# Kernel tuning notes

Measured on AMD Instinct MI355X. Metric: run time of the kernel, lower is better.

## Reference

```python
import jax, jax.numpy as jnp
import numpy as np

KS = 3          # kernel_size
DIM = 3         # dimension
B, N = 4, 16384
CMAX = 64       # voxel coordinate range [0, CMAX)
K = KS ** DIM   # kernel_volume = 27
SHIFT = KS      # makes neighbor coords non-negative
BASE = CMAX + 2 * KS  # per-axis encoding base


def _kernel_offsets():
    # matches torch: arange(-ks//2 + 1, ks//2 + 1) per dim, meshgrid 'ij'
    r = jnp.arange(-(KS) // 2 + 1, KS // 2 + 1)
    grid = jnp.meshgrid(*([r] * DIM), indexing='ij')
    return jnp.stack(grid, axis=-1).reshape(-1, DIM)  # [K, DIM]


def setup_inputs() -> dict:
    key = jax.random.key(0)
    k1, _ = jax.random.split(key)
    coordinates = jax.random.randint(k1, (B, N, DIM), 0, CMAX, dtype=jnp.int32)
    batch_indices = jnp.broadcast_to(jnp.arange(B, dtype=jnp.int32)[:, None], (B, N))
    return {"coordinates": coordinates, "batch_indices": batch_indices}


def reference(coordinates, batch_indices):
    """Vectorized kernel-map construction (replaces the Python dict-hash loops).

    Returns:
      in_idx  [B*N*K] : index of the input point within its batch
      out_idx [B*N*K] : dense output index (first-appearance order, matches dict insertion)
      rel_pos [B*N*K] : kernel offset index
      out_key [B*N*K, 3] : unique output coordinates, padded with -1 past num_out
      num_out [] : number of valid unique output keys
    """
    Bv, Nv, D = coordinates.shape
    offsets = _kernel_offsets()            # [K, 3]
    Kv = offsets.shape[0]
    # neighbor coordinates, iteration order (b, idx, k) == torch loop order
    nb = coordinates[:, :, None, :] + offsets[None, None, :, :]  # [B, N, K, 3]
    c = nb + SHIFT                                               # non-negative
    b_ids = batch_indices[:, :, None].astype(jnp.int32)
    keys = (b_ids * (BASE ** 3)
            + (c[..., 0] * BASE + c[..., 1]) * BASE + c[..., 2]).reshape(-1)  # [T]
    T = keys.shape[0]
    sentinel = jnp.int32(Bv * (BASE ** 3))  # > any real key
    uniq, first_idx, inv = jnp.unique(keys, size=T, fill_value=sentinel,
                                      return_index=True, return_inverse=True)
    valid = uniq != sentinel
    # recover first-appearance (dict-insertion) order from sorted-unique
    first_adj = jnp.where(valid, first_idx, T)
    order = jnp.argsort(first_adj)                      # insertion order -> sorted pos
    rank = jnp.zeros((T,), dtype=jnp.int32).at[order].set(jnp.arange(T, dtype=jnp.int32))
    out_idx = rank[inv]                                 # [T] dense output indices
    # decode unique keys back to (x, y, z) in insertion order
    uo = uniq[order]
    vo = valid[order]
    rem = uo % (BASE ** 3)
    x = rem // (BASE * BASE) - SHIFT
    y = (rem // BASE) % BASE - SHIFT
    z = rem % BASE - SHIFT
    out_key = jnp.where(vo[:, None], jnp.stack([x, y, z], axis=-1), -1)  # [T, 3]
    num_out = vo.sum()
    in_idx = jnp.tile(jnp.repeat(jnp.arange(Nv, dtype=jnp.int32), Kv), Bv)
    rel_pos = jnp.tile(jnp.arange(Kv, dtype=jnp.int32), Bv * Nv)
    return in_idx, out_idx, rel_pos, out_key, num_out
```

## Files before the change

### kernel.cpp

```cpp
#include <hip/hip_runtime.h>

namespace {
constexpr int Bc   = 4;
constexpr int Nc   = 16384;
constexpr int Kc   = 27;
constexpr int Pc   = 68;
constexpr int P2c  = Pc * Pc;
constexpr int P3c  = Pc * P2c;
constexpr int NPts = Bc * Nc;
constexpr int Tc   = NPts * Kc;
constexpr int FT   = Bc * P3c;
constexpr unsigned INFu = 0xFFFFFFFFu;
constexpr int PLANES = Bc * Pc;
constexpr int PBLKS  = 1024;
constexpr int PPTS   = NPts / PBLKS;
}

__device__ __forceinline__ unsigned min3u(unsigned a, unsigned b, unsigned c) {
    return min(min(a, b), c);
}
__device__ __forceinline__ int cidx(int bb, int x, int y, int z) {
    return bb * P3c + ((x + 2) * Pc + (y + 2)) * Pc + (z + 2);
}

__global__ void __launch_bounds__(256)
k0_init(unsigned* __restrict__ cm) {
    const int g = blockIdx.x * 256 + threadIdx.x;
    const uint4 iv = make_uint4(INFu, INFu, INFu, INFu);
    const int n4 = FT / 4;
    for (int i = g; i < n4; i += 256 * 256)
        reinterpret_cast<uint4*>(cm)[i] = iv;
}

__global__ void __launch_bounds__(256)
k1_atomic_easy(const int* __restrict__ coords, const int* __restrict__ batch,
               unsigned* __restrict__ cm,
               int* __restrict__ in_idx, int* __restrict__ rel_pos) {
    const int g = blockIdx.x * 256 + threadIdx.x;
    if (g < NPts) {
        const int bb = batch[g];
        const int x = coords[3 * g], y = coords[3 * g + 1], z = coords[3 * g + 2];
        atomicMin(&cm[cidx(bb, x, y, z)], (unsigned)(g & (Nc - 1)));
    }
    const int t = 4 * g;
    int4 a, r;
    a.x = (t / Kc) & (Nc - 1);       r.x = t % Kc;
    a.y = ((t + 1) / Kc) & (Nc - 1); r.y = (t + 1) % Kc;
    a.z = ((t + 2) / Kc) & (Nc - 1); r.z = (t + 2) % Kc;
    a.w = ((t + 3) / Kc) & (Nc - 1); r.w = (t + 3) % Kc;
    reinterpret_cast<int4*>(in_idx)[g]  = a;
    reinterpret_cast<int4*>(rel_pos)[g] = r;
}

__global__ void __launch_bounds__(256)
k2_planes(const unsigned* __restrict__ cm, unsigned* __restrict__ Btab) {
    __shared__ unsigned s0[P2c];
    __shared__ unsigned s1[P2c];
    const int tid = threadIdx.x;
    const int base = blockIdx.x * P2c;
    for (int i4 = tid; i4 < P2c / 4; i4 += 256)
        reinterpret_cast<uint4*>(s0)[i4] =
            reinterpret_cast<const uint4*>(cm + base)[i4];
    __syncthreads();
    for (int i = tid; i < P2c; i += 256) {
        const int col = i % Pc;
        unsigned v = INFu;
        if (col >= 1 && col <= 66) v = min3u(s0[i - 1], s0[i], s0[i + 1]);
        s1[i] = v;
    }
    __syncthreads();
    for (int i = tid; i < P2c; i += 256) {
        const int row = i / Pc;
        unsigned v = INFu;
        if (row >= 1 && row <= 66) v = min3u(s1[i - Pc], s1[i], s1[i + Pc]);
        Btab[base + i] = v;
    }
}

__global__ void __launch_bounds__(256)
k3_pred(const int* __restrict__ coords, const int* __restrict__ batch,
        const unsigned* __restrict__ Btab,
        int* __restrict__ owners, unsigned long long* __restrict__ packed,
        int* __restrict__ blockSums) {
    __shared__ int parts[PPTS][4];
    __shared__ int pbs[PPTS];
    __shared__ int scn[256];
    const int tid = threadIdx.x, bid = blockIdx.x;
    const int p = tid >> 2, j = tid & 3;
    const int pt = bid * PPTS + p;

    int mypb = 0;
    if (j < 3) {
        const unsigned uidx = (unsigned)(pt & (Nc - 1));
        const int bb = batch[pt];
        const int x = coords[3 * pt], y = coords[3 * pt + 1],
                  z = coords[3 * pt + 2];
        const unsigned* basep =
            Btab + bb * P3c + (x * Pc + (y + j + 1)) * Pc + (z + 1);
        unsigned w[5][3];
        #pragma unroll
        for (int xi = 0; xi < 5; ++xi) {
            const unsigned* q = basep + xi * P2c;
            w[xi][0] = q[0]; w[xi][1] = q[1]; w[xi][2] = q[2];
        }
        #pragma unroll
        for (int dxl = 0; dxl < 3; ++dxl)
            #pragma unroll
            for (int dz = 0; dz < 3; ++dz) {
                const unsigned m = min3u(w[dxl][dz], w[dxl + 1][dz],
                                         w[dxl + 2][dz]);
                const int kk = (dxl * 3 + j) * 3 + dz;
                owners[pt * Kc + kk] = (int)m;
                mypb |= (m == uidx) ? (1 << kk) : 0;
            }
    }
    parts[p][j] = mypb;
    __syncthreads();
    if (j == 0) pbs[p] = parts[p][0] | parts[p][1] | parts[p][2];
    __syncthreads();

    const int v = (tid < PPTS) ? __popc(pbs[tid]) : 0;
    scn[tid] = v;
    __syncthreads();
    #pragma unroll
    for (int off = 1; off < PPTS; off <<= 1) {
        int u = (tid >= off) ? scn[tid - off] : 0;
        __syncthreads();
        scn[tid] += u;
        __syncthreads();
    }
    if (tid < PPTS) {
        const int intra = scn[tid] - v;
        const int ptw = bid * PPTS + tid;
        packed[ptw] = (unsigned long long)(unsigned)pbs[tid]
                    | ((unsigned long long)(unsigned)intra << 27);
    }
    if (tid == PPTS - 1) blockSums[bid] = scn[PPTS - 1];
}

__global__ void __launch_bounds__(256)
k4_outputs(const int* __restrict__ coords, const int* __restrict__ batch,
           const int* __restrict__ owners,
           const unsigned long long* __restrict__ packed,
           const int* __restrict__ blockSums,
           int* __restrict__ out_idx, int* __restrict__ out_key,
           int* __restrict__ num_out) {
    __shared__ int pref[PBLKS];
    __shared__ int scn[256];
    __shared__ int s_total;
    const int tid = threadIdx.x, bid = blockIdx.x;

    const int4 bsv = reinterpret_cast<const int4*>(blockSums)[tid];
    const int s = bsv.x + bsv.y + bsv.z + bsv.w;
    scn[tid] = s;
    __syncthreads();
    #pragma unroll
    for (int off = 1; off < 256; off <<= 1) {
        int u = (tid >= off) ? scn[tid - off] : 0;
        __syncthreads();
        scn[tid] += u;
        __syncthreads();
    }
    const int excl = scn[tid] - s;
    pref[4 * tid + 0] = excl;
    pref[4 * tid + 1] = excl + bsv.x;
    pref[4 * tid + 2] = excl + bsv.x + bsv.y;
    pref[4 * tid + 3] = excl + bsv.x + bsv.y + bsv.z;
    if (tid == 255) s_total = scn[255];
    __syncthreads();

    const int t  = bid * 256 + tid;
    const int pt = t / Kc;
    const int k  = t - Kc * pt;
    const int bb = batch[pt];
    const int x = coords[3 * pt], y = coords[3 * pt + 1], z = coords[3 * pt + 2];
    const int dx = k / 9 - 1;
    const int dy = (k / 3) % 3 - 1;
    const int dz = k - (k / 3) * 3 - 1;
    const int cx = x + dx, cy = y + dy, cz = z + dz;

    const int o  = owners[t];
    const int go = bb * Nc + o;
    const int ox = coords[3 * go], oy = coords[3 * go + 1],
              oz = coords[3 * go + 2];
    const int kp = (cx - ox + 1) * 9 + (cy - oy + 1) * 3 + (cz - oz + 1);
    const unsigned long long pk = packed[go];
    const int pbo    = (int)(pk & 0x7ffffffull);
    const int intrao = (int)(pk >> 27);
    out_idx[t] = pref[go >> 6] + intrao + __popc(pbo & ((1 << kp) - 1));

    const unsigned long long pkw = packed[pt];
    const int pbw = (int)(pkw & 0x7ffffffull);
    if ((pbw >> k) & 1) {
        const int r = pref[pt >> 6] + (int)(pkw >> 27)
                    + __popc(pbw & ((1 << k) - 1));
        out_key[3 * r + 0] = cx;
        out_key[3 * r + 1] = cy;
        out_key[3 * r + 2] = cz;
    }
    if (t >= s_total) {
        out_key[3 * t + 0] = -1;
        out_key[3 * t + 1] = -1;
        out_key[3 * t + 2] = -1;
    }
    if (t == 0) num_out[0] = s_total;
}

extern "C" void kernel_launch(void* const* d_in, const int* in_sizes, int n_in,
                              void* d_out, int out_size, void* d_ws, size_t ws_size,
                              hipStream_t stream) {
    const int* coords = (const int*)d_in[0];
    const int* batch  = (const int*)d_in[1];
    int* out = (int*)d_out;
    int* in_idx  = out;
    int* out_idx = out + Tc;
    int* rel_pos = out + 2 * Tc;
    int* out_key = out + 3 * Tc;
    int* num_out = out + 6 * Tc;

    unsigned* ws = (unsigned*)d_ws;
    unsigned* cm   = ws;
    unsigned* Btab = ws + FT;
    unsigned long long* packed =
        (unsigned long long*)(ws + 2 * FT);
    int* owners    = (int*)(packed + NPts);
    int* blockSums = owners + Tc;

    k0_init<<<256, 256, 0, stream>>>(cm);
    k1_atomic_easy<<<Tc / 4 / 256, 256, 0, stream>>>(coords, batch, cm,
                                                     in_idx, rel_pos);
    k2_planes<<<PLANES, 256, 0, stream>>>(cm, Btab);
    k3_pred<<<PBLKS, 256, 0, stream>>>(coords, batch, Btab,
                                       owners, packed, blockSums);
    k4_outputs<<<Tc / 256, 256, 0, stream>>>(coords, batch, owners, packed,
                                             blockSums, out_idx, out_key,
                                             num_out);
}
```

Measured before the change: 106.7 us.

## Drop plane-min pass, pack coords, shrink owners, chunk output kernel

Removes the separate plane min-filter kernel and computes the y/z min-filter directly from the atomic-min grid inside the prediction kernel. Coordinates are packed into one 32-bit word and stored alongside the bitmask and prefix in the packed array, so the output kernel no longer gathers coords or batch indices. Owner indices are stored as 16-bit values to halve that traffic. The output kernel now handles four chunks per block, so each block's blockSums prefix scan is amortized over more elements. The trade-off is more redundant loads and min operations per point in the prediction kernel.

```diff
diff --git a/kernel.cpp b/kernel.cpp
--- a/kernel.cpp
+++ b/kernel.cpp
@@ -11,16 +11,14 @@
 constexpr int Tc   = NPts * Kc;
 constexpr int FT   = Bc * P3c;
 constexpr unsigned INFu = 0xFFFFFFFFu;
-constexpr int PLANES = Bc * Pc;
 constexpr int PBLKS  = 1024;
 constexpr int PPTS   = NPts / PBLKS;
+constexpr int OBLKS  = 1728;
+constexpr int OCHUNK = 4;
 }
 
 __device__ __forceinline__ unsigned min3u(unsigned a, unsigned b, unsigned c) {
     return min(min(a, b), c);
-}
-__device__ __forceinline__ int cidx(int bb, int x, int y, int z) {
-    return bb * P3c + ((x + 2) * Pc + (y + 2)) * Pc + (z + 2);
 }
 
 __global__ void __launch_bounds__(256)
@@ -28,19 +26,21 @@
     const int g = blockIdx.x * 256 + threadIdx.x;
     const uint4 iv = make_uint4(INFu, INFu, INFu, INFu);
     const int n4 = FT / 4;
-    for (int i = g; i < n4; i += 256 * 256)
+    for (int i = g; i < n4; i += 512 * 256)
         reinterpret_cast<uint4*>(cm)[i] = iv;
 }
 
 __global__ void __launch_bounds__(256)
 k1_atomic_easy(const int* __restrict__ coords, const int* __restrict__ batch,
-               unsigned* __restrict__ cm,
+               unsigned* __restrict__ cm, unsigned* __restrict__ pcoord,
                int* __restrict__ in_idx, int* __restrict__ rel_pos) {
     const int g = blockIdx.x * 256 + threadIdx.x;
     if (g < NPts) {
         const int bb = batch[g];
         const int x = coords[3 * g], y = coords[3 * g + 1], z = coords[3 * g + 2];
-        atomicMin(&cm[cidx(bb, x, y, z)], (unsigned)(g & (Nc - 1)));
+        pcoord[g] = (unsigned)(x | (y << 6) | (z << 12) | (bb << 18));
+        atomicMin(&cm[bb * P3c + (x + 2) * P2c + (y + 2) * Pc + (z + 2)],
+                  (unsigned)(g & (Nc - 1)));
     }
     const int t = 4 * g;
     int4 a, r;
@@ -53,35 +53,9 @@
 }
 
 __global__ void __launch_bounds__(256)
-k2_planes(const unsigned* __restrict__ cm, unsigned* __restrict__ Btab) {
-    __shared__ unsigned s0[P2c];
-    __shared__ unsigned s1[P2c];
-    const int tid = threadIdx.x;
-    const int base = blockIdx.x * P2c;
-    for (int i4 = tid; i4 < P2c / 4; i4 += 256)
-        reinterpret_cast<uint4*>(s0)[i4] =
-            reinterpret_cast<const uint4*>(cm + base)[i4];
-    __syncthreads();
-    for (int i = tid; i < P2c; i += 256) {
-        const int col = i % Pc;
-        unsigned v = INFu;
-        if (col >= 1 && col <= 66) v = min3u(s0[i - 1], s0[i], s0[i + 1]);
-        s1[i] = v;
-    }
-    __syncthreads();
-    for (int i = tid; i < P2c; i += 256) {
-        const int row = i / Pc;
-        unsigned v = INFu;
-        if (row >= 1 && row <= 66) v = min3u(s1[i - Pc], s1[i], s1[i + Pc]);
-        Btab[base + i] = v;
-    }
-}
-
-__global__ void __launch_bounds__(256)
-k3_pred(const int* __restrict__ coords, const int* __restrict__ batch,
-        const unsigned* __restrict__ Btab,
-        int* __restrict__ owners, unsigned long long* __restrict__ packed,
-        int* __restrict__ blockSums) {
+k3_pred(const unsigned* __restrict__ pcoord, const unsigned* __restrict__ cm,
+        unsigned short* __restrict__ owners,
+        unsigned long long* __restrict__ packed, int* __restrict__ blockSums) {
     __shared__ int parts[PPTS][4];
     __shared__ int pbs[PPTS];
     __shared__ int scn[256];
@@ -91,17 +65,28 @@
 
     int mypb = 0;
     if (j < 3) {
+        const unsigned pc = pcoord[pt];
+        const int x = pc & 63, y = (pc >> 6) & 63, z = (pc >> 12) & 63,
+                  bb = pc >> 18;
         const unsigned uidx = (unsigned)(pt & (Nc - 1));
-        const int bb = batch[pt];
-        const int x = coords[3 * pt], y = coords[3 * pt + 1],
-                  z = coords[3 * pt + 2];
-        const unsigned* basep =
-            Btab + bb * P3c + (x * Pc + (y + j + 1)) * Pc + (z + 1);
+        const unsigned* base0 = cm + bb * P3c + x * P2c + (y + j) * Pc + z;
         unsigned w[5][3];
         #pragma unroll
         for (int xi = 0; xi < 5; ++xi) {
-            const unsigned* q = basep + xi * P2c;
-            w[xi][0] = q[0]; w[xi][1] = q[1]; w[xi][2] = q[2];
+            const unsigned* q = base0 + xi * P2c;
+            unsigned rz[3][3];
+            #pragma unroll
+            for (int yy = 0; yy < 3; ++yy) {
+                const unsigned* qq = q + yy * Pc;
+                const unsigned v0 = qq[0], v1 = qq[1], v2 = qq[2],
+                               v3 = qq[3], v4 = qq[4];
+                rz[yy][0] = min3u(v0, v1, v2);
+                rz[yy][1] = min3u(v1, v2, v3);
+                rz[yy][2] = min3u(v2, v3, v4);
+            }
+            #pragma unroll
+            for (int dz = 0; dz < 3; ++dz)
+                w[xi][dz] = min3u(rz[0][dz], rz[1][dz], rz[2][dz]);
         }
         #pragma unroll
         for (int dxl = 0; dxl < 3; ++dxl)
@@ -110,7 +95,7 @@
                 const unsigned m = min3u(w[dxl][dz], w[dxl + 1][dz],
                                          w[dxl + 2][dz]);
                 const int kk = (dxl * 3 + j) * 3 + dz;
-                owners[pt * Kc + kk] = (int)m;
+                owners[pt * Kc + kk] = (unsigned short)m;
                 mypb |= (m == uidx) ? (1 << kk) : 0;
             }
     }
@@ -131,16 +116,16 @@
     }
     if (tid < PPTS) {
         const int intra = scn[tid] - v;
-        const int ptw = bid * PPTS + tid;
-        packed[ptw] = (unsigned long long)(unsigned)pbs[tid]
-                    | ((unsigned long long)(unsigned)intra << 27);
+        packed[bid * PPTS + tid] =
+            (unsigned long long)(unsigned)pbs[tid]
+          | ((unsigned long long)(unsigned)intra << 27)
+          | ((unsigned long long)pcoord[bid * PPTS + tid] << 38);
     }
     if (tid == PPTS - 1) blockSums[bid] = scn[PPTS - 1];
 }
 
 __global__ void __launch_bounds__(256)
-k4_outputs(const int* __restrict__ coords, const int* __restrict__ batch,
-           const int* __restrict__ owners,
+k4_outputs(const unsigned short* __restrict__ owners,
            const unsigned long long* __restrict__ packed,
            const int* __restrict__ blockSums,
            int* __restrict__ out_idx, int* __restrict__ out_key,
@@ -169,41 +154,47 @@
     if (tid == 255) s_total = scn[255];
     __syncthreads();
 
-    const int t  = bid * 256 + tid;
-    const int pt = t / Kc;
-    const int k  = t - Kc * pt;
-    const int bb = batch[pt];
-    const int x = coords[3 * pt], y = coords[3 * pt + 1], z = coords[3 * pt + 2];
-    const int dx = k / 9 - 1;
-    const int dy = (k / 3) % 3 - 1;
-    const int dz = k - (k / 3) * 3 - 1;
-    const int cx = x + dx, cy = y + dy, cz = z + dz;
-
-    const int o  = owners[t];
-    const int go = bb * Nc + o;
-    const int ox = coords[3 * go], oy = coords[3 * go + 1],
-              oz = coords[3 * go + 2];
-    const int kp = (cx - ox + 1) * 9 + (cy - oy + 1) * 3 + (cz - oz + 1);
-    const unsigned long long pk = packed[go];
-    const int pbo    = (int)(pk & 0x7ffffffull);
-    const int intrao = (int)(pk >> 27);
-    out_idx[t] = pref[go >> 6] + intrao + __popc(pbo & ((1 << kp) - 1));
-
-    const unsigned long long pkw = packed[pt];
-    const int pbw = (int)(pkw & 0x7ffffffull);
-    if ((pbw >> k) & 1) {
-        const int r = pref[pt >> 6] + (int)(pkw >> 27)
-                    + __popc(pbw & ((1 << k) - 1));
-        out_key[3 * r + 0] = cx;
-        out_key[3 * r + 1] = cy;
-        out_key[3 * r + 2] = cz;
-    }
-    if (t >= s_total) {
-        out_key[3 * t + 0] = -1;
-        out_key[3 * t + 1] = -1;
-        out_key[3 * t + 2] = -1;
-    }
-    if (t == 0) num_out[0] = s_total;
+    const int total = s_total;
+    #pragma unroll
+    for (int c = 0; c < OCHUNK; ++c) {
+        const int t  = bid * (256 * OCHUNK) + c * 256 + tid;
+        const int pt = t / Kc;
+        const int k  = t - Kc * pt;
+
+        const unsigned long long pkw = packed[pt];
+        const int pbw    = (int)(pkw & 0x7ffffffull);
+        const int intraw = (int)((pkw >> 27) & 0x7ffull);
+        const unsigned pcw = (unsigned)(pkw >> 38);
+        const int x = pcw & 63, y = (pcw >> 6) & 63, z = (pcw >> 12) & 63,
+                  bb = pcw >> 18;
+        const int dx = k / 9 - 1;
+        const int dy = (k / 3) % 3 - 1;
+        const int dz = k - (k / 3) * 3 - 1;
+        const int cx = x + dx, cy = y + dy, cz = z + dz;
+
+        const int o  = (int)owners[t];
+        const int go = bb * Nc + o;
+        const unsigned long long pko = packed[go];
+        const int pbo    = (int)(pko & 0x7ffffffull);
+        const int intrao = (int)((pko >> 27) & 0x7ffull);
+        const unsigned pco = (unsigned)(pko >> 38);
+        const int ox = pco & 63, oy = (pco >> 6) & 63, oz = (pco >> 12) & 63;
+        const int kp = (cx - ox + 1) * 9 + (cy - oy + 1) * 3 + (cz - oz + 1);
+        out_idx[t] = pref[go >> 6] + intrao + __popc(pbo & ((1 << kp) - 1));
+
+        if ((pbw >> k) & 1) {
+            const int r = pref[pt >> 6] + intraw + __popc(pbw & ((1 << k) - 1));
+            out_key[3 * r + 0] = cx;
+            out_key[3 * r + 1] = cy;
+            out_key[3 * r + 2] = cz;
+        }
+        if (t >= total) {
+            out_key[3 * t + 0] = -1;
+            out_key[3 * t + 1] = -1;
+            out_key[3 * t + 2] = -1;
+        }
+        if (t == 0) num_out[0] = total;
+    }
 }
 
 extern "C" void kernel_launch(void* const* d_in, const int* in_sizes, int n_in,
@@ -219,20 +210,18 @@
     int* num_out = out + 6 * Tc;
 
     unsigned* ws = (unsigned*)d_ws;
-    unsigned* cm   = ws;
-    unsigned* Btab = ws + FT;
+    unsigned* cm = ws;
     unsigned long long* packed =
-        (unsigned long long*)(ws + 2 * FT);
-    int* owners    = (int*)(packed + NPts);
-    int* blockSums = owners + Tc;
-
-    k0_init<<<256, 256, 0, stream>>>(cm);
-    k1_atomic_easy<<<Tc / 4 / 256, 256, 0, stream>>>(coords, batch, cm,
+        (unsigned long long*)(ws + FT);
+    unsigned short* owners =
+        (unsigned short*)(packed + NPts);
+    int* blockSums = (int*)(owners + Tc);
+    unsigned* pcoord = (unsigned*)(blockSums + PBLKS);
+
+    k0_init<<<512, 256, 0, stream>>>(cm);
+    k1_atomic_easy<<<Tc / 4 / 256, 256, 0, stream>>>(coords, batch, cm, pcoord,
                                                      in_idx, rel_pos);
-    k2_planes<<<PLANES, 256, 0, stream>>>(cm, Btab);
-    k3_pred<<<PBLKS, 256, 0, stream>>>(coords, batch, Btab,
-                                       owners, packed, blockSums);
-    k4_outputs<<<Tc / 256, 256, 0, stream>>>(coords, batch, owners, packed,
-                                             blockSums, out_idx, out_key,
-                                             num_out);
-}
+    k3_pred<<<PBLKS, 256, 0, stream>>>(pcoord, cm, owners, packed, blockSums);
+    k4_outputs<<<OBLKS, 256, 0, stream>>>(owners, packed, blockSums,
+                                          out_idx, out_key, num_out);
+}
```

New measurement: 105.5 us. Within noise of the previous version (-1.1%).
